# Kernel tuning notes

Measured on AMD Instinct MI355X. Metric: run time of the kernel, lower is better.

## Reference

```python
import jax, jax.numpy as jnp
import numpy as np

HEADS = 16
TOPK = 2048  # dsa_topk


def setup_inputs() -> dict:
    key = jax.random.key(0)
    ks = jax.random.split(key, 9)
    B, Q, KV, C = 2, 2048, 16384, 1024
    w = lambda k: jax.random.normal(k, (C, C), dtype=jnp.float32) * 0.02
    return {
        "hidden_states": jax.random.normal(ks[0], (B, Q, C), dtype=jnp.float32),
        "encoder_hidden_states": jax.random.normal(ks[1], (B, KV, C), dtype=jnp.float32),
        "Wq": w(ks[2]),
        "Wk": w(ks[3]),
        "Wv": w(ks[4]),
        "Wo": w(ks[5]),
        "bo": jnp.zeros((C,), dtype=jnp.float32),
        "Wg": jax.random.normal(ks[6], (C, C), dtype=jnp.float32) * 0.01,  # xavier gain 0.1
        "bg": jnp.full((C,), -1.5, dtype=jnp.float32),  # gate_init_bias
    }


def reference(hidden_states, encoder_hidden_states, Wq, Wk, Wv, Wo, bo, Wg, bg):
    B, Q, C = hidden_states.shape
    H = HEADS
    D = C // H
    scale = 1.0 / jnp.sqrt(jnp.asarray(D, dtype=hidden_states.dtype))

    # projections -> [B, H, S, D]
    q = (hidden_states @ Wq).reshape(B, Q, H, D).transpose(0, 2, 1, 3)
    k = (encoder_hidden_states @ Wk).reshape(B, -1, H, D).transpose(0, 2, 1, 3)
    v = (encoder_hidden_states @ Wv).reshape(B, -1, H, D).transpose(0, 2, 1, 3)

    # _sparse_select: query-summary scored top-k KV gather (kv_len > TOPK here)
    q_summary = q.mean(axis=2)                                   # [B, H, D]
    sel_score = jnp.einsum("bhd,bhkd->bhk", q_summary, k) * scale
    idx = jax.lax.top_k(sel_score, TOPK)[1]                      # [B, H, TOPK]
    k_sel = jnp.take_along_axis(k, idx[..., None], axis=2)       # [B, H, TOPK, D]
    v_sel = jnp.take_along_axis(v, idx[..., None], axis=2)

    # attention over selected KV
    scores = jnp.einsum("bhqd,bhkd->bhqk", q, k_sel) * scale
    probs = jax.nn.softmax(scores.astype(jnp.float32), axis=-1).astype(scores.dtype)
    out = jnp.einsum("bhqk,bhkd->bhqd", probs, v_sel)
    out = out.transpose(0, 2, 1, 3).reshape(B, Q, C)

    # sigmoid gate + output projection (to_out[1] dropout is identity at eval)
    out = out * jax.nn.sigmoid(out @ Wg + bg)
    out = out @ Wo + bo

    # residual_connection=True, rescale_output_factor=1.0
    return out + hidden_states
```

## Files before the change

kernel.cpp:

```cpp
#include <hip/hip_runtime.h>
#include <hip/hip_bf16.h>

typedef unsigned short u16;
typedef __bf16 bf16x8 __attribute__((ext_vector_type(8)));
typedef float f32x4 __attribute__((ext_vector_type(4)));

__device__ __forceinline__ u16 f2bf(float f) {
    union { float f; unsigned int u; } v; v.f = f;
    unsigned int u = v.u;
    unsigned int r = (u + 0x7fffu + ((u >> 16) & 1u)) >> 16;
    return (u16)r;
}
__device__ __forceinline__ float bf2f(u16 b) {
    union { unsigned int u; float f; } v; v.u = ((unsigned int)b) << 16;
    return v.f;
}

__device__ __forceinline__ void glds16(const u16* g, u16* l) {
    __builtin_amdgcn_global_load_lds(
        (__attribute__((address_space(1))) void*)(g),
        (__attribute__((address_space(3))) void*)(l), 16, 0, 0);
}

__global__ __launch_bounds__(256) void cast_bf16_kernel(const float* __restrict__ src,
                                                        u16* __restrict__ dst, int n4) {
    int i = blockIdx.x * 256 + threadIdx.x;
    if (i >= n4) return;
    float4 v = ((const float4*)src)[i];
    ushort4 o;
    o.x = f2bf(v.x); o.y = f2bf(v.y); o.z = f2bf(v.z); o.w = f2bf(v.w);
    ((ushort4*)dst)[i] = o;
}

__global__ __launch_bounds__(256) void transpose_cast_kernel(
    const float* __restrict__ Wq, const float* __restrict__ Wk, const float* __restrict__ Wv,
    const float* __restrict__ Wg, const float* __restrict__ Wo,
    u16* __restrict__ WqT, u16* __restrict__ WkvT, u16* __restrict__ WgT, u16* __restrict__ WoT) {
    __shared__ float tile[32][33];
    const float* src; u16* dst;
    switch (blockIdx.z) {
        case 0: src = Wq; dst = WqT; break;
        case 1: src = Wk; dst = WkvT; break;
        case 2: src = Wv; dst = WkvT + (size_t)1024 * 1024; break;
        case 3: src = Wg; dst = WgT; break;
        default: src = Wo; dst = WoT; break;
    }
    int n0 = blockIdx.x * 32, k0 = blockIdx.y * 32;
    int tx = threadIdx.x, ty = threadIdx.y;
    #pragma unroll
    for (int j = 0; j < 4; j++)
        tile[ty + j * 8][tx] = src[(size_t)(k0 + ty + j * 8) * 1024 + n0 + tx];
    __syncthreads();
    #pragma unroll
    for (int j = 0; j < 4; j++)
        dst[(size_t)(n0 + ty + j * 8) * 1024 + k0 + tx] = f2bf(tile[tx][ty + j * 8]);
}

template <int EPI>
__global__ __launch_bounds__(256) void gemm_bf16(
    const u16* __restrict__ A, const u16* __restrict__ B, int ldc,
    u16* __restrict__ Cbf, const float* __restrict__ bias,
    const u16* __restrict__ mul_src, const float* __restrict__ add_src,
    float* __restrict__ Cf) {
    constexpr int K = 1024;
    const int tid = threadIdx.x;
    const int w = tid >> 6, l = tid & 63;
    const int lr = l & 15, lg = l >> 4;
    const int wr = w >> 1, wc = w & 1;
    const int m0 = blockIdx.y * 128, n0 = blockIdx.x * 128;

    __shared__ u16 As[128 * 64];
    __shared__ u16 Bs[128 * 64];

    const f32x4 fz = {0.f, 0.f, 0.f, 0.f};
    f32x4 acc[4][4];
    #pragma unroll
    for (int i = 0; i < 4; i++)
        #pragma unroll
        for (int j = 0; j < 4; j++) acc[i][j] = fz;

    const int lane_row = l >> 3;
    const int lane_sl  = l & 7;
    const int src_ch   = lane_sl ^ lane_row;
    const u16* Ab = A + (size_t)(m0 + w * 32 + lane_row) * K + src_ch * 8;
    const u16* Bb = B + (size_t)(n0 + w * 32 + lane_row) * K + src_ch * 8;

    for (int kt = 0; kt < K; kt += 64) {
        __syncthreads();
        #pragma unroll
        for (int j = 0; j < 4; j++) {
            glds16(Ab + (size_t)j * 8 * K + kt, As + (w * 32 + j * 8) * 64);
            glds16(Bb + (size_t)j * 8 * K + kt, Bs + (w * 32 + j * 8) * 64);
        }
        __syncthreads();
        #pragma unroll
        for (int kk = 0; kk < 2; kk++) {
            bf16x8 af[4], bfr[4];
            #pragma unroll
            for (int mi = 0; mi < 4; mi++) {
                int row = wr * 64 + mi * 16 + lr;
                int ch = (kk * 4 + lg) ^ (row & 7);
                af[mi] = *(const bf16x8*)(As + row * 64 + ch * 8);
            }
            #pragma unroll
            for (int ni = 0; ni < 4; ni++) {
                int row = wc * 64 + ni * 16 + lr;
                int ch = (kk * 4 + lg) ^ (row & 7);
                bfr[ni] = *(const bf16x8*)(Bs + row * 64 + ch * 8);
            }
            #pragma unroll
            for (int mi = 0; mi < 4; mi++)
                #pragma unroll
                for (int ni = 0; ni < 4; ni++)
                    acc[mi][ni] = __builtin_amdgcn_mfma_f32_16x16x32_bf16(
                        af[mi], bfr[ni], acc[mi][ni], 0, 0, 0);
        }
    }

    #pragma unroll
    for (int mi = 0; mi < 4; mi++) {
        #pragma unroll
        for (int ni = 0; ni < 4; ni++) {
            #pragma unroll
            for (int r = 0; r < 4; r++) {
                int gm = m0 + wr * 64 + mi * 16 + lg * 4 + r;
                int gn = n0 + wc * 64 + ni * 16 + lr;
                float v = acc[mi][ni][r];
                if (EPI == 0) {
                    Cbf[(size_t)gm * ldc + gn] = f2bf(v);
                } else if (EPI == 2) {
                    float g = v + bias[gn];
                    float a = bf2f(mul_src[(size_t)gm * ldc + gn]);
                    float sg = 1.f / (1.f + __expf(-g));
                    Cbf[(size_t)gm * ldc + gn] = f2bf(a * sg);
                } else {
                    Cf[(size_t)gm * ldc + gn] = v + bias[gn] + add_src[(size_t)gm * ldc + gn];
                }
            }
        }
    }
}

__global__ __launch_bounds__(256) void hsum1_kernel(const float* __restrict__ hidden,
                                                    float* __restrict__ part) {
    int b = blockIdx.x, chunk = blockIdx.y;
    int tid = threadIdx.x;
    const float4* src = (const float4*)(hidden + ((size_t)b * 2048 + chunk * 16) * 1024) + tid;
    float4 acc = {0.f, 0.f, 0.f, 0.f};
    #pragma unroll
    for (int r = 0; r < 16; r++) {
        float4 v = src[r * 256];
        acc.x += v.x; acc.y += v.y; acc.z += v.z; acc.w += v.w;
    }
    ((float4*)(part + ((size_t)b * 128 + chunk) * 1024))[tid] = acc;
}

__global__ __launch_bounds__(256) void hsum2_kernel(const float* __restrict__ part,
                                                    float* __restrict__ hm) {
    int b = blockIdx.x, tid = threadIdx.x;
    const float4* src = (const float4*)(part + (size_t)b * 128 * 1024) + tid;
    float4 acc = {0.f, 0.f, 0.f, 0.f};
    for (int c = 0; c < 128; c++) {
        float4 v = src[c * 256];
        acc.x += v.x; acc.y += v.y; acc.z += v.z; acc.w += v.w;
    }
    const float inv = 1.f / 2048.f;
    acc.x *= inv; acc.y *= inv; acc.z *= inv; acc.w *= inv;
    ((float4*)(hm + (size_t)b * 1024))[tid] = acc;
}

__global__ __launch_bounds__(256) void qz_kernel(const float* __restrict__ hm,
                                                 const u16* __restrict__ WqT,
                                                 const u16* __restrict__ WkT,
                                                 u16* __restrict__ z_bf) {
    int bh = blockIdx.x, b = bh >> 4, h = bh & 15;
    int tid = threadIdx.x;
    __shared__ float hm_l[1024];
    __shared__ float qs_l[64];
    __shared__ float red[256];
    ((float4*)hm_l)[tid] = ((const float4*)(hm + (size_t)b * 1024))[tid];
    __syncthreads();
    {
        int d = tid >> 2, q = tid & 3;
        const u16* wq = WqT + (size_t)(h * 64 + d) * 1024 + q * 256;
        float a = 0.f;
        for (int i = 0; i < 256; i += 8) {
            uint4 u = *(const uint4*)(wq + i);
            const u16* p = (const u16*)&u;
            #pragma unroll
            for (int j = 0; j < 8; j++) a += bf2f(p[j]) * hm_l[q * 256 + i + j];
        }
        red[tid] = a;
    }
    __syncthreads();
    if (tid < 64)
        qs_l[tid] = red[tid * 4] + red[tid * 4 + 1] + red[tid * 4 + 2] + red[tid * 4 + 3];
    __syncthreads();
    {
        float z0 = 0.f, z1 = 0.f, z2 = 0.f, z3 = 0.f;
        for (int d = 0; d < 64; d++) {
            float qs = qs_l[d];
            const u16* wk = WkT + (size_t)(h * 64 + d) * 1024 + tid * 4;
            uint2 u = *(const uint2*)wk;
            const u16* p = (const u16*)&u;
            z0 += qs * bf2f(p[0]); z1 += qs * bf2f(p[1]);
            z2 += qs * bf2f(p[2]); z3 += qs * bf2f(p[3]);
        }
        ushort4 o;
        o.x = f2bf(z0); o.y = f2bf(z1); o.z = f2bf(z2); o.w = f2bf(z3);
        *(ushort4*)(z_bf + (size_t)bh * 1024 + tid * 4) = o;
    }
}

__global__ __launch_bounds__(256) void score_mfma_kernel(const u16* __restrict__ ebf,
                                                         const u16* __restrict__ z_bf,
                                                         float* __restrict__ score) {
    const int b = blockIdx.y, kv0 = blockIdx.x * 256;
    const int tid = threadIdx.x, w = tid >> 6, l = tid & 63;
    const int lr = l & 15, lg = l >> 4;
    __shared__ u16 z_lds[16 * 1024];
    __shared__ u16 e_lds[256 * 64];
    {
        int row = tid >> 4, cg = tid & 15;
        const u16* src = z_bf + (size_t)(b * 16 + row) * 1024 + cg * 64;
        #pragma unroll
        for (int i = 0; i < 8; i++) {
            uint4 u = *(const uint4*)(src + i * 8);
            int ch = cg * 8 + i;
            *(uint4*)(z_lds + row * 1024 + (ch ^ (row & 7)) * 8) = u;
        }
    }
    const int lane_row = l >> 3, src_ch = (l & 7) ^ lane_row;
    const f32x4 fz = {0.f, 0.f, 0.f, 0.f};
    f32x4 acc[4];
    #pragma unroll
    for (int ni = 0; ni < 4; ni++) acc[ni] = fz;

    for (int kt = 0; kt < 1024; kt += 64) {
        __syncthreads();
        #pragma unroll
        for (int j = 0; j < 8; j++) {
            const u16* src = ebf + (size_t)(b * 16384 + kv0 + w * 64 + j * 8 + lane_row) * 1024 + kt + src_ch * 8;
            glds16(src, e_lds + (w * 64 + j * 8) * 64);
        }
        __syncthreads();
        #pragma unroll
        for (int ks = 0; ks < 2; ks++) {
            int chg = (kt >> 3) + ks * 4 + lg;
            bf16x8 af = *(const bf16x8*)(z_lds + lr * 1024 + (chg ^ (lr & 7)) * 8);
            #pragma unroll
            for (int ni = 0; ni < 4; ni++) {
                int row = w * 64 + ni * 16 + lr;
                bf16x8 bf_ = *(const bf16x8*)(e_lds + row * 64 + (((ks * 4 + lg) ^ (lr & 7))) * 8);
                acc[ni] = __builtin_amdgcn_mfma_f32_16x16x32_bf16(af, bf_, acc[ni], 0, 0, 0);
            }
        }
    }
    #pragma unroll
    for (int ni = 0; ni < 4; ni++)
        #pragma unroll
        for (int r = 0; r < 4; r++)
            score[(size_t)(b * 16 + lg * 4 + r) * 16384 + kv0 + w * 64 + ni * 16 + lr] = acc[ni][r];
}

__global__ __launch_bounds__(1024) void select_kernel(const float* __restrict__ score,
                                                      int* __restrict__ sel_idx) {
    const int bh = blockIdx.x;
    const float* sc = score + (size_t)bh * 16384;
    const int tid = threadIdx.x;
    const int grp = tid >> 8;

    __shared__ int hist[4][256];
    __shared__ int total[256];
    __shared__ int bc[4];

    u16 key[16];
    #pragma unroll
    for (int j = 0; j < 16; j++) {
        unsigned int b = __float_as_uint(sc[tid + j * 1024]);
        unsigned int ui = (b & 0x80000000u) ? ~b : (b | 0x80000000u);
        key[j] = (u16)(ui >> 16);
    }

    ((int*)hist)[tid] = 0;
    __syncthreads();
    #pragma unroll
    for (int j = 0; j < 16; j++) atomicAdd(&hist[grp][key[j] >> 8], 1);
    __syncthreads();
    if (tid < 256) total[tid] = hist[0][tid] + hist[1][tid] + hist[2][tid] + hist[3][tid];
    __syncthreads();
    if (tid == 0) {
        int want = 2048, acc = 0;
        for (int dd = 255; dd >= 0; dd--) {
            acc += total[dd];
            if (acc >= want) { bc[0] = dd; bc[1] = want - (acc - total[dd]); break; }
        }
    }
    __syncthreads();
    const int hi = bc[0];
    const int want1 = bc[1];

    ((int*)hist)[tid] = 0;
    __syncthreads();
    #pragma unroll
    for (int j = 0; j < 16; j++)
        if ((key[j] >> 8) == hi) atomicAdd(&hist[grp][key[j] & 0xff], 1);
    __syncthreads();
    if (tid < 256) total[tid] = hist[0][tid] + hist[1][tid] + hist[2][tid] + hist[3][tid];
    __syncthreads();
    if (tid == 0) {
        int want = want1, acc = 0;
        for (int dd = 255; dd >= 0; dd--) {
            acc += total[dd];
            if (acc >= want) { bc[0] = (hi << 8) | dd; bc[1] = want - (acc - total[dd]); break; }
        }
        bc[2] = 0; bc[3] = 0;
    }
    __syncthreads();
    const u16 thr = (u16)bc[0];
    const int n_eq = bc[1];
    const int base_eq = 2048 - n_eq;

    int* out = sel_idx + (size_t)bh * 2048;
    #pragma unroll
    for (int j = 0; j < 16; j++) {
        int i = tid + j * 1024;
        if (key[j] > thr) {
            int p = atomicAdd(&bc[2], 1);
            out[p] = i;
        } else if (key[j] == thr) {
            int p = atomicAdd(&bc[3], 1);
            if (p < n_eq) out[base_eq + p] = i;
        }
    }
}

__global__ __launch_bounds__(256) void selproj_kernel(const u16* __restrict__ ebf,
                                                      const u16* __restrict__ WkvT,
                                                      const int* __restrict__ sel_idx,
                                                      u16* __restrict__ k_sel,
                                                      u16* __restrict__ v_selT) {
    const int bh = blockIdx.y, b = bh >> 4, h = bh & 15;
    const int t0 = blockIdx.x * 128;
    const int tid = threadIdx.x, w = tid >> 6, l = tid & 63;
    const int lr = l & 15, lg = l >> 4;
    const int lane_row = l >> 3, src_ch = (l & 7) ^ lane_row;

    __shared__ u16 e_lds[128 * 64];
    __shared__ u16 w_lds[128 * 64];

    int encrow[4], wrow[4];
    #pragma unroll
    for (int j = 0; j < 4; j++) {
        int t = t0 + w * 32 + j * 8 + lane_row;
        encrow[j] = b * 16384 + sel_idx[(size_t)bh * 2048 + t];
        int r = w * 32 + j * 8 + lane_row;
        wrow[j] = (r < 64) ? (h * 64 + r) : (1024 + h * 64 + (r & 63));
    }

    const f32x4 fz = {0.f, 0.f, 0.f, 0.f};
    f32x4 acc_k[2][4], acc_v[8];
    #pragma unroll
    for (int i = 0; i < 2; i++)
        #pragma unroll
        for (int j = 0; j < 4; j++) acc_k[i][j] = fz;
    #pragma unroll
    for (int i = 0; i < 8; i++) acc_v[i] = fz;

    for (int kt = 0; kt < 1024; kt += 64) {
        __syncthreads();
        #pragma unroll
        for (int j = 0; j < 4; j++) {
            glds16(ebf + (size_t)encrow[j] * 1024 + kt + src_ch * 8, e_lds + (w * 32 + j * 8) * 64);
            glds16(WkvT + (size_t)wrow[j] * 1024 + kt + src_ch * 8, w_lds + (w * 32 + j * 8) * 64);
        }
        __syncthreads();
        #pragma unroll
        for (int ks = 0; ks < 2; ks++) {
            bf16x8 ae[2];
            #pragma unroll
            for (int mi = 0; mi < 2; mi++) {
                int row = w * 32 + mi * 16 + lr;
                ae[mi] = *(const bf16x8*)(e_lds + row * 64 + (((ks * 4 + lg) ^ (row & 7))) * 8);
            }
            bf16x8 aw;
            {
                int row = 64 + w * 16 + lr;
                aw = *(const bf16x8*)(w_lds + row * 64 + (((ks * 4 + lg) ^ (row & 7))) * 8);
            }
            #pragma unroll
            for (int ni = 0; ni < 4; ni++) {
                int row = ni * 16 + lr;
                bf16x8 bw = *(const bf16x8*)(w_lds + row * 64 + (((ks * 4 + lg) ^ (row & 7))) * 8);
                acc_k[0][ni] = __builtin_amdgcn_mfma_f32_16x16x32_bf16(ae[0], bw, acc_k[0][ni], 0, 0, 0);
                acc_k[1][ni] = __builtin_amdgcn_mfma_f32_16x16x32_bf16(ae[1], bw, acc_k[1][ni], 0, 0, 0);
            }
            #pragma unroll
            for (int ni = 0; ni < 8; ni++) {
                int row = ni * 16 + lr;
                bf16x8 be = *(const bf16x8*)(e_lds + row * 64 + (((ks * 4 + lg) ^ (row & 7))) * 8);
                acc_v[ni] = __builtin_amdgcn_mfma_f32_16x16x32_bf16(aw, be, acc_v[ni], 0, 0, 0);
            }
        }
    }

    u16* kb = k_sel + (size_t)bh * 2048 * 64;
    #pragma unroll
    for (int mi = 0; mi < 2; mi++)
        #pragma unroll
        for (int ni = 0; ni < 4; ni++)
            #pragma unroll
            for (int r = 0; r < 4; r++) {
                int t = t0 + w * 32 + mi * 16 + lg * 4 + r;
                int d = ni * 16 + lr;
                kb[(size_t)t * 64 + (((d >> 3) ^ (t & 7)) * 8) + (d & 7)] = f2bf(acc_k[mi][ni][r]);
            }
    u16* vb = v_selT + (size_t)bh * 64 * 2048;
    #pragma unroll
    for (int ni = 0; ni < 8; ni++)
        #pragma unroll
        for (int r = 0; r < 4; r++) {
            int d = w * 16 + lg * 4 + r;
            int t = t0 + ni * 16 + lr;
            int tl = t & 63;
            vb[(size_t)d * 2048 + (t & ~63) + ((((tl >> 3) ^ (d & 7))) * 8) + (tl & 7)] =
                f2bf(acc_v[ni][r]);
        }
}

__global__ __launch_bounds__(256) void attn_kernel(
    const u16* __restrict__ q_bf, const u16* __restrict__ k_sel,
    const u16* __restrict__ v_selT, u16* __restrict__ attn_out) {
    const int bh = blockIdx.y, b = bh >> 4, h = bh & 15;
    const int q0 = blockIdx.x * 64;
    const int tid = threadIdx.x, w = tid >> 6, l = tid & 63;
    const int lr = l & 15, lg = l >> 4;
    const int lk = lr & 7;
    const float SC = 0.18033688011f;
    const float THR = 11.0f;

    __shared__ u16 k_lds[2][64 * 64];
    __shared__ u16 vt_lds[64 * 64];
    __shared__ __bf16 p_lds[4][16][68];

    const u16* qb = q_bf + ((size_t)b * 2048 + q0 + w * 16 + lr) * 1024 + h * 64;
    bf16x8 qf0 = *(const bf16x8*)(qb + lg * 8);
    bf16x8 qf1 = *(const bf16x8*)(qb + 32 + lg * 8);

    const f32x4 fz = {0.f, 0.f, 0.f, 0.f};
    f32x4 o[4];
    #pragma unroll
    for (int f = 0; f < 4; f++) o[f] = fz;
    float mm = -1e30f;
    float l_part[4] = {0.f, 0.f, 0.f, 0.f};

    const u16* kb  = k_sel + (size_t)bh * 2048 * 64;
    const u16* vtb = v_selT + (size_t)bh * 64 * 2048;

    auto stageK = [&](int it, int buf) {
        const u16* ksrc = kb + (size_t)(it * 64 + w * 16) * 64 + (size_t)l * 8;
        glds16(ksrc,       k_lds[buf] + (w * 16) * 64);
        glds16(ksrc + 512, k_lds[buf] + (w * 16 + 8) * 64);
    };
    auto stageV = [&](int it) {
        const u16* vsrc = vtb + (size_t)(w * 16 + (l >> 3)) * 2048 + it * 64 + (l & 7) * 8;
        glds16(vsrc,            vt_lds + (w * 16) * 64);
        glds16(vsrc + 8 * 2048, vt_lds + (w * 16 + 8) * 64);
    };

    stageK(0, 0);
    __syncthreads();

    #pragma unroll 1
    for (int it = 0; it < 32; ++it) {
        const int cur = it & 1;
        stageV(it);
        if (it + 1 < 32) stageK(it + 1, cur ^ 1);

        f32x4 s[4];
        #pragma unroll
        for (int c = 0; c < 4; c++) s[c] = fz;
        __builtin_amdgcn_s_setprio(1);
        #pragma unroll
        for (int c = 0; c < 4; c++) {
            const u16* krow = k_lds[cur] + (c * 16 + lr) * 64;
            bf16x8 kf0 = *(const bf16x8*)(krow + (lg ^ lk) * 8);
            s[c] = __builtin_amdgcn_mfma_f32_16x16x32_bf16(qf0, kf0, s[c], 0, 0, 0);
            bf16x8 kf1 = *(const bf16x8*)(krow + (((4 + lg) ^ lk)) * 8);
            s[c] = __builtin_amdgcn_mfma_f32_16x16x32_bf16(qf1, kf1, s[c], 0, 0, 0);
        }
        __builtin_amdgcn_s_setprio(0);

        float mx = s[0][0];
        #pragma unroll
        for (int c = 0; c < 4; c++)
            #pragma unroll
            for (int r = 0; r < 4; r++) mx = fmaxf(mx, s[c][r]);
        mx = fmaxf(mx, __shfl_xor(mx, 1));
        mx = fmaxf(mx, __shfl_xor(mx, 2));
        mx = fmaxf(mx, __shfl_xor(mx, 4));
        mx = fmaxf(mx, __shfl_xor(mx, 8));
        mx = fmaxf(mx, __shfl_xor(mx, 16));
        mx = fmaxf(mx, __shfl_xor(mx, 32));
        mx *= SC;
        if (mx > mm + THR) {
            float al = __builtin_amdgcn_exp2f(mm - mx);
            mm = mx;
            #pragma unroll
            for (int r = 0; r < 4; r++) l_part[r] *= al;
            #pragma unroll
            for (int f = 0; f < 4; f++)
                #pragma unroll
                for (int r = 0; r < 4; r++) o[f][r] *= al;
        }
        #pragma unroll
        for (int c = 0; c < 4; c++) {
            #pragma unroll
            for (int r = 0; r < 4; r++) {
                float p = __builtin_amdgcn_exp2f(__builtin_fmaf(s[c][r], SC, -mm));
                l_part[r] += p;
                p_lds[w][lg * 4 + r][c * 16 + lr] = (__bf16)p;
            }
        }

        if (it + 1 < 32) {
            asm volatile("s_waitcnt vmcnt(2)" ::: "memory");
        } else {
            asm volatile("s_waitcnt vmcnt(0)" ::: "memory");
        }
        __builtin_amdgcn_sched_barrier(0);
        __builtin_amdgcn_s_barrier();

        __builtin_amdgcn_s_setprio(1);
        #pragma unroll
        for (int kk = 0; kk < 2; kk++) {
            bf16x8 ap = *(const bf16x8*)(&p_lds[w][lr][kk * 32 + lg * 8]);
            #pragma unroll
            for (int f = 0; f < 4; f++) {
                const u16* vrow = vt_lds + (f * 16 + lr) * 64;
                bf16x8 bv = *(const bf16x8*)(vrow + (((kk * 4 + lg) ^ lk)) * 8);
                o[f] = __builtin_amdgcn_mfma_f32_16x16x32_bf16(ap, bv, o[f], 0, 0, 0);
            }
        }
        __builtin_amdgcn_s_setprio(0);

        __syncthreads();
    }

    float invl[4];
    #pragma unroll
    for (int r = 0; r < 4; r++) {
        float lr_ = l_part[r];
        lr_ += __shfl_xor(lr_, 1);
        lr_ += __shfl_xor(lr_, 2);
        lr_ += __shfl_xor(lr_, 4);
        lr_ += __shfl_xor(lr_, 8);
        invl[r] = 1.f / lr_;
    }
    u16* ob = attn_out + ((size_t)b * 2048 + q0 + w * 16 + lg * 4) * 1024 + h * 64 + lr;
    #pragma unroll
    for (int f = 0; f < 4; f++) {
        #pragma unroll
        for (int r = 0; r < 4; r++) {
            __bf16 hv = (__bf16)(o[f][r] * invl[r]);
            ob[(size_t)r * 1024 + f * 16] = *(u16*)&hv;
        }
    }
}

extern "C" void kernel_launch(void* const* d_in, const int* in_sizes, int n_in,
                              void* d_out, int out_size, void* d_ws, size_t ws_size,
                              hipStream_t stream) {
    const float* hidden = (const float*)d_in[0];
    const float* enc    = (const float*)d_in[1];
    const float* Wq = (const float*)d_in[2];
    const float* Wk = (const float*)d_in[3];
    const float* Wv = (const float*)d_in[4];
    const float* Wo = (const float*)d_in[5];
    const float* bo = (const float*)d_in[6];
    const float* Wg = (const float*)d_in[7];
    const float* bg = (const float*)d_in[8];
    float* out = (float*)d_out;

    char* ws = (char*)d_ws;
    size_t off = 0;
    auto alloc = [&](size_t bytes) -> char* {
        char* p = ws + off;
        off += (bytes + 255) & ~(size_t)255;
        return p;
    };
    u16* hbf   = (u16*)alloc(4096ull * 1024 * 2);
    u16* ebf   = (u16*)alloc(32768ull * 1024 * 2);
    u16* WqT   = (u16*)alloc(1024ull * 1024 * 2);
    u16* WkvT  = (u16*)alloc(2048ull * 1024 * 2);
    u16* WgT   = (u16*)alloc(1024ull * 1024 * 2);
    u16* WoT   = (u16*)alloc(1024ull * 1024 * 2);
    u16* q_bf  = (u16*)alloc(4096ull * 1024 * 2);
    float* hm  = (float*)alloc(2ull * 1024 * 4);
    float* part = (float*)alloc(2ull * 128 * 1024 * 4);
    u16* z_bf  = (u16*)alloc(32ull * 1024 * 2);
    float* scor = (float*)alloc(32ull * 16384 * 4);
    int* sel    = (int*)alloc(32ull * 2048 * 4);
    u16* ksel   = (u16*)alloc(32ull * 2048 * 64 * 2);
    u16* vT     = (u16*)alloc(32ull * 64 * 2048 * 2);
    u16* attn   = (u16*)alloc(4096ull * 1024 * 2);
    u16* gate   = (u16*)alloc(4096ull * 1024 * 2);
    (void)ws_size; (void)in_sizes; (void)n_in; (void)out_size;

    hsum1_kernel<<<dim3(2, 128), 256, 0, stream>>>(hidden, part);
    hsum2_kernel<<<2, 256, 0, stream>>>(part, hm);
    cast_bf16_kernel<<<4096, 256, 0, stream>>>(hidden, hbf, 1048576);
    cast_bf16_kernel<<<32768, 256, 0, stream>>>(enc, ebf, 8388608);
    transpose_cast_kernel<<<dim3(32, 32, 5), dim3(32, 8), 0, stream>>>(
        Wq, Wk, Wv, Wg, Wo, WqT, WkvT, WgT, WoT);

    qz_kernel<<<32, 256, 0, stream>>>(hm, WqT, WkvT, z_bf);
    score_mfma_kernel<<<dim3(64, 2), 256, 0, stream>>>(ebf, z_bf, scor);
    select_kernel<<<32, 1024, 0, stream>>>(scor, sel);
    selproj_kernel<<<dim3(16, 32), 256, 0, stream>>>(ebf, WkvT, sel, ksel, vT);

    gemm_bf16<0><<<dim3(8, 32), 256, 0, stream>>>(hbf, WqT, 1024, q_bf, nullptr, nullptr, nullptr, nullptr);
    attn_kernel<<<dim3(32, 32), 256, 0, stream>>>(q_bf, ksel, vT, attn);

    gemm_bf16<2><<<dim3(8, 32), 256, 0, stream>>>(attn, WgT, 1024, gate, bg, attn, nullptr, nullptr);
    gemm_bf16<3><<<dim3(8, 32), 256, 0, stream>>>(gate, WoT, 1024, nullptr, bo, nullptr, hidden, out);
}
```

Measured before the change: 275.4 us.

## Fuse encoder bf16 cast into selection scoring; widen attention blocks to eight waves

The separate fp32-to-bf16 cast of the encoder states is removed and done inside the selection-score kernel. That kernel loads fp32 tiles, converts them, writes them to LDS for the MFMA and also writes the bf16 copy to global memory for the later gather, which saves one full read of the bf16 encoder tensor. The attention kernel now runs 512 threads over 128 queries per block, so each K/V tile staged in LDS is shared by twice as many waves. The P matrix is written as packed ushort4 stores, with a matching permuted V-transpose layout produced in selproj. The score kernel's fp32 loads are register-prefetched but need extra barriers, and the larger attention block may lower occupancy.

After: 254.0 us. 1.08x faster.

```diff
diff --git a/kernel.cpp b/kernel.cpp
--- a/kernel.cpp
+++ b/kernel.cpp
@@ -212,14 +212,15 @@
     }
 }
 
-__global__ __launch_bounds__(256) void score_mfma_kernel(const u16* __restrict__ ebf,
-                                                         const u16* __restrict__ z_bf,
-                                                         float* __restrict__ score) {
-    const int b = blockIdx.y, kv0 = blockIdx.x * 256;
+__global__ __launch_bounds__(256) void escore_kernel(const float* __restrict__ enc,
+                                                     const u16* __restrict__ z_bf,
+                                                     u16* __restrict__ ebf,
+                                                     float* __restrict__ score) {
+    const int b = blockIdx.y, kv0 = blockIdx.x * 128;
     const int tid = threadIdx.x, w = tid >> 6, l = tid & 63;
     const int lr = l & 15, lg = l >> 4;
     __shared__ u16 z_lds[16 * 1024];
-    __shared__ u16 e_lds[256 * 64];
+    __shared__ u16 e_lds[128 * 64];
     {
         int row = tid >> 4, cg = tid & 15;
         const u16* src = z_bf + (size_t)(b * 16 + row) * 1024 + cg * 64;
@@ -230,37 +231,58 @@
             *(uint4*)(z_lds + row * 1024 + (ch ^ (row & 7)) * 8) = u;
         }
     }
-    const int lane_row = l >> 3, src_ch = (l & 7) ^ lane_row;
+    const int rbase = tid >> 4;
+    const int cgrp  = tid & 15;
+    const float* ebase = enc + (size_t)(b * 16384 + kv0) * 1024;
+    u16* obase = ebf + (size_t)(b * 16384 + kv0) * 1024;
+
+    float4 rv[8];
+    auto loadT = [&](int kt) {
+        #pragma unroll
+        for (int jj = 0; jj < 8; jj++) {
+            int row = rbase + jj * 16;
+            rv[jj] = *(const float4*)(ebase + (size_t)row * 1024 + kt + cgrp * 4);
+        }
+    };
+    loadT(0);
+
     const f32x4 fz = {0.f, 0.f, 0.f, 0.f};
-    f32x4 acc[4];
-    #pragma unroll
-    for (int ni = 0; ni < 4; ni++) acc[ni] = fz;
+    f32x4 acc[2];
+    acc[0] = fz; acc[1] = fz;
+    __syncthreads();
 
     for (int kt = 0; kt < 1024; kt += 64) {
+        #pragma unroll
+        for (int jj = 0; jj < 8; jj++) {
+            int row = rbase + jj * 16;
+            ushort4 pk;
+            pk.x = f2bf(rv[jj].x); pk.y = f2bf(rv[jj].y);
+            pk.z = f2bf(rv[jj].z); pk.w = f2bf(rv[jj].w);
+            int ch = cgrp >> 1;
+            int off = ((ch ^ (row & 7)) * 8) + ((cgrp & 1) * 4);
+            *(ushort4*)(e_lds + row * 64 + off) = pk;
+            *(ushort4*)(obase + (size_t)row * 1024 + kt + cgrp * 4) = pk;
+        }
         __syncthreads();
-        #pragma unroll
-        for (int j = 0; j < 8; j++) {
-            const u16* src = ebf + (size_t)(b * 16384 + kv0 + w * 64 + j * 8 + lane_row) * 1024 + kt + src_ch * 8;
-            glds16(src, e_lds + (w * 64 + j * 8) * 64);
-        }
-        __syncthreads();
+        if (kt + 64 < 1024) loadT(kt + 64);
         #pragma unroll
         for (int ks = 0; ks < 2; ks++) {
             int chg = (kt >> 3) + ks * 4 + lg;
             bf16x8 af = *(const bf16x8*)(z_lds + lr * 1024 + (chg ^ (lr & 7)) * 8);
             #pragma unroll
-            for (int ni = 0; ni < 4; ni++) {
-                int row = w * 64 + ni * 16 + lr;
+            for (int ni = 0; ni < 2; ni++) {
+                int row = w * 32 + ni * 16 + lr;
                 bf16x8 bf_ = *(const bf16x8*)(e_lds + row * 64 + (((ks * 4 + lg) ^ (lr & 7))) * 8);
                 acc[ni] = __builtin_amdgcn_mfma_f32_16x16x32_bf16(af, bf_, acc[ni], 0, 0, 0);
             }
         }
-    }
-    #pragma unroll
-    for (int ni = 0; ni < 4; ni++)
+        __syncthreads();
+    }
+    #pragma unroll
+    for (int ni = 0; ni < 2; ni++)
         #pragma unroll
         for (int r = 0; r < 4; r++)
-            score[(size_t)(b * 16 + lg * 4 + r) * 16384 + kv0 + w * 64 + ni * 16 + lr] = acc[ni][r];
+            score[(size_t)(b * 16 + lg * 4 + r) * 16384 + kv0 + w * 32 + ni * 16 + lr] = acc[ni][r];
 }
 
 __global__ __launch_bounds__(1024) void select_kernel(const float* __restrict__ score,
@@ -423,16 +445,17 @@
             int d = w * 16 + lg * 4 + r;
             int t = t0 + ni * 16 + lr;
             int tl = t & 63;
-            vb[(size_t)d * 2048 + (t & ~63) + ((((tl >> 3) ^ (d & 7))) * 8) + (tl & 7)] =
+            int kap = (tl & 15) * 4 + (tl >> 4);
+            vb[(size_t)d * 2048 + (t & ~63) + (((kap >> 3) ^ (d & 7)) * 8) + (kap & 7)] =
                 f2bf(acc_v[ni][r]);
         }
 }
 
-__global__ __launch_bounds__(256) void attn_kernel(
+__global__ __launch_bounds__(512) void attn_kernel(
     const u16* __restrict__ q_bf, const u16* __restrict__ k_sel,
     const u16* __restrict__ v_selT, u16* __restrict__ attn_out) {
     const int bh = blockIdx.y, b = bh >> 4, h = bh & 15;
-    const int q0 = blockIdx.x * 64;
+    const int q0 = blockIdx.x * 128;
     const int tid = threadIdx.x, w = tid >> 6, l = tid & 63;
     const int lr = l & 15, lg = l >> 4;
     const int lk = lr & 7;
@@ -441,7 +464,7 @@
 
     __shared__ u16 k_lds[2][64 * 64];
     __shared__ u16 vt_lds[64 * 64];
-    __shared__ __bf16 p_lds[4][16][68];
+    __shared__ u16 p_lds[8][16][68];
 
     const u16* qb = q_bf + ((size_t)b * 2048 + q0 + w * 16 + lr) * 1024 + h * 64;
     bf16x8 qf0 = *(const bf16x8*)(qb + lg * 8);
@@ -458,14 +481,12 @@
     const u16* vtb = v_selT + (size_t)bh * 64 * 2048;
 
     auto stageK = [&](int it, int buf) {
-        const u16* ksrc = kb + (size_t)(it * 64 + w * 16) * 64 + (size_t)l * 8;
-        glds16(ksrc,       k_lds[buf] + (w * 16) * 64);
-        glds16(ksrc + 512, k_lds[buf] + (w * 16 + 8) * 64);
+        const u16* ksrc = kb + (size_t)(it * 64 + w * 8) * 64 + (size_t)l * 8;
+        glds16(ksrc, k_lds[buf] + (w * 8) * 64);
     };
     auto stageV = [&](int it) {
-        const u16* vsrc = vtb + (size_t)(w * 16 + (l >> 3)) * 2048 + it * 64 + (l & 7) * 8;
-        glds16(vsrc,            vt_lds + (w * 16) * 64);
-        glds16(vsrc + 8 * 2048, vt_lds + (w * 16 + 8) * 64);
+        const u16* vsrc = vtb + (size_t)(w * 8 + (l >> 3)) * 2048 + it * 64 + (l & 7) * 8;
+        glds16(vsrc, vt_lds + (w * 8) * 64);
     };
 
     stageK(0, 0);
@@ -514,17 +535,22 @@
                 for (int r = 0; r < 4; r++) o[f][r] *= al;
         }
         #pragma unroll
-        for (int c = 0; c < 4; c++) {
-            #pragma unroll
-            for (int r = 0; r < 4; r++) {
+        for (int r = 0; r < 4; r++) {
+            ushort4 pk;
+            u16 pb[4];
+            #pragma unroll
+            for (int c = 0; c < 4; c++) {
                 float p = __builtin_amdgcn_exp2f(__builtin_fmaf(s[c][r], SC, -mm));
                 l_part[r] += p;
-                p_lds[w][lg * 4 + r][c * 16 + lr] = (__bf16)p;
-            }
+                __bf16 hv = (__bf16)p;
+                pb[c] = *(u16*)&hv;
+            }
+            pk.x = pb[0]; pk.y = pb[1]; pk.z = pb[2]; pk.w = pb[3];
+            *(ushort4*)(&p_lds[w][lg * 4 + r][lr * 4]) = pk;
         }
 
         if (it + 1 < 32) {
-            asm volatile("s_waitcnt vmcnt(2)" ::: "memory");
+            asm volatile("s_waitcnt vmcnt(1)" ::: "memory");
         } else {
             asm volatile("s_waitcnt vmcnt(0)" ::: "memory");
         }
@@ -610,17 +636,16 @@
     hsum1_kernel<<<dim3(2, 128), 256, 0, stream>>>(hidden, part);
     hsum2_kernel<<<2, 256, 0, stream>>>(part, hm);
     cast_bf16_kernel<<<4096, 256, 0, stream>>>(hidden, hbf, 1048576);
-    cast_bf16_kernel<<<32768, 256, 0, stream>>>(enc, ebf, 8388608);
     transpose_cast_kernel<<<dim3(32, 32, 5), dim3(32, 8), 0, stream>>>(
         Wq, Wk, Wv, Wg, Wo, WqT, WkvT, WgT, WoT);
 
     qz_kernel<<<32, 256, 0, stream>>>(hm, WqT, WkvT, z_bf);
-    score_mfma_kernel<<<dim3(64, 2), 256, 0, stream>>>(ebf, z_bf, scor);
+    escore_kernel<<<dim3(128, 2), 256, 0, stream>>>(enc, z_bf, ebf, scor);
     select_kernel<<<32, 1024, 0, stream>>>(scor, sel);
     selproj_kernel<<<dim3(16, 32), 256, 0, stream>>>(ebf, WkvT, sel, ksel, vT);
 
     gemm_bf16<0><<<dim3(8, 32), 256, 0, stream>>>(hbf, WqT, 1024, q_bf, nullptr, nullptr, nullptr, nullptr);
-    attn_kernel<<<dim3(32, 32), 256, 0, stream>>>(q_bf, ksel, vT, attn);
+    attn_kernel<<<dim3(16, 32), 512, 0, stream>>>(q_bf, ksel, vT, attn);
 
     gemm_bf16<2><<<dim3(8, 32), 256, 0, stream>>>(attn, WgT, 1024, gate, bg, attn, nullptr, nullptr);
     gemm_bf16<3><<<dim3(8, 32), 256, 0, stream>>>(gate, WoT, 1024, nullptr, bo, nullptr, hidden, out);
```
